# Kernel optimization log

Hardware: AMD Instinct MI355X
Metric: run time of the kernel (lower is better)

The kernel has to match this reference:

```python
import jax, jax.numpy as jnp
import numpy as np

N = 1_000_000
FEAT_DIM = 256
N_CLASS = 345
N_DOMAIN = 6
BETA = 0.5
EPS = 1e-5


def setup_inputs() -> dict:
    key = jax.random.key(0)
    k1, k2, k3, k4 = jax.random.split(key, 4)
    feats = jax.random.normal(k1, (N, FEAT_DIM), dtype=jnp.float32)
    mean = jax.random.normal(k2, (N_DOMAIN, N_CLASS, FEAT_DIM), dtype=jnp.float32)
    amount = jnp.zeros((N_DOMAIN, N_CLASS), dtype=jnp.float32)
    labels = jax.random.randint(k3, (N,), 0, N_CLASS, dtype=jnp.int64 if jax.config.jax_enable_x64 else jnp.int32)
    domains = jax.random.randint(k4, (N,), 0, N_DOMAIN, dtype=jnp.int64 if jax.config.jax_enable_x64 else jnp.int32)
    return {"feats": feats, "mean": mean, "amount": amount,
            "labels": labels, "domains": domains}


def reference(feats, mean, amount, labels, domains):
    # Segmented per-(domain, class) mean of feats. Equivalent to the original
    # onehot broadcast-multiply + sum, but without the O(N*C*F) intermediate.
    seg = domains * N_CLASS + labels  # [N]
    sums = jax.ops.segment_sum(feats, seg, num_segments=N_DOMAIN * N_CLASS)
    sums = sums.reshape(N_DOMAIN, N_CLASS, FEAT_DIM)
    counts = jax.ops.segment_sum(jnp.ones((feats.shape[0],), dtype=feats.dtype), seg,
                                 num_segments=N_DOMAIN * N_CLASS)
    counts = counts.reshape(N_DOMAIN, N_CLASS)

    tmp_mean = sums / (counts[..., None] + EPS)  # [D, C, F]
    # Mask of (domain, class) cells actually observed (tmp_mean row nonzero)
    tmp_mask = (jnp.sum(tmp_mean, axis=-1) != 0).astype(feats.dtype)[..., None]  # [D, C, 1]

    new_mean = mean * (1.0 - tmp_mask) + (mean * BETA + tmp_mean * (1.0 - BETA)) * tmp_mask
    new_amount = jnp.where(counts > 0, jnp.ones_like(amount), amount)
    return new_mean, new_amount
```

## Files before the change

kernel.cpp:

```cpp
#include <hip/hip_runtime.h>
#include <stddef.h>

constexpr int FEAT = 256;
constexpr int F4   = FEAT / 4;
constexpr int NCLS = 345;
constexpr int NDOM = 6;
constexpr int NSEG = NCLS * NDOM;
constexpr int SB   = 256;
constexpr int ITILE = 1024;
constexpr float BETA = 0.5f;
constexpr float EPS  = 1e-5f;

typedef float f32x4 __attribute__((ext_vector_type(4)));

__global__ void __launch_bounds__(256)
k_seg_hist(const int* __restrict__ labels, const int* __restrict__ domains,
           int n, int chunk, int* __restrict__ seg, int* __restrict__ W) {
    __shared__ int h[NSEG];
    for (int i = threadIdx.x; i < NSEG; i += blockDim.x) h[i] = 0;
    __syncthreads();
    const int b  = blockIdx.x;
    const int lo = b * chunk;
    const int hi = min(n, lo + chunk);
    for (int i = lo + threadIdx.x; i < hi; i += blockDim.x) {
        int s = domains[i] * NCLS + labels[i];
        seg[i] = s;
        atomicAdd(&h[s], 1);
    }
    __syncthreads();
    int* Wb = W + (size_t)b * NSEG;
    for (int i = threadIdx.x; i < NSEG; i += blockDim.x) Wb[i] = h[i];
}

__global__ void k_totals(const int* __restrict__ W, int* __restrict__ totals) {
    const int s = blockIdx.x;
    const int t = threadIdx.x;
    int sum = 0;
    for (int b = t; b < SB; b += 64) sum += W[(size_t)b * NSEG + s];
    for (int off = 1; off < 64; off <<= 1) sum += __shfl_xor(sum, off, 64);
    if (t == 0) totals[s] = sum;
}

__global__ void k_scan(const int* __restrict__ totals, int* __restrict__ offsets,
                       int* __restrict__ ticket) {
    constexpr int T  = 256;
    constexpr int CH = (NSEG + T - 1) / T;
    __shared__ int csum[T];
    int t = threadIdx.x;
    if (t == 0) ticket[0] = 0;
    int base = t * CH;
    int sum = 0;
    for (int j = 0; j < CH; ++j) {
        int idx = base + j;
        if (idx < NSEG) sum += totals[idx];
    }
    csum[t] = sum;
    __syncthreads();
    for (int off = 1; off < T; off <<= 1) {
        int v = (t >= off) ? csum[t - off] : 0;
        __syncthreads();
        csum[t] += v;
        __syncthreads();
    }
    int run = csum[t] - sum;
    for (int j = 0; j < CH; ++j) {
        int idx = base + j;
        if (idx < NSEG) {
            offsets[idx] = run;
            run += totals[idx];
        }
    }
}

__global__ void __launch_bounds__(256)
k_bases(const int* __restrict__ W, const int* __restrict__ offsets,
        int* __restrict__ Bmat) {
    const int s = blockIdx.x;
    const int t = threadIdx.x;
    __shared__ int sc[SB];
    int w = W[(size_t)t * NSEG + s];
    sc[t] = w;
    __syncthreads();
    for (int off = 1; off < SB; off <<= 1) {
        int v = (t >= off) ? sc[t - off] : 0;
        __syncthreads();
        sc[t] += v;
        __syncthreads();
    }
    Bmat[(size_t)t * NSEG + s] = offsets[s] + (sc[t] - w);
}

__global__ void __launch_bounds__(256)
k_scatter(const int* __restrict__ seg, int n, int chunk,
          const int* __restrict__ Bmat, int* __restrict__ sorted) {
    __shared__ int cur[NSEG];
    const int b = blockIdx.x;
    const int* Bb = Bmat + (size_t)b * NSEG;
    for (int i = threadIdx.x; i < NSEG; i += blockDim.x) cur[i] = Bb[i];
    __syncthreads();
    const int lo = b * chunk;
    const int hi = min(n, lo + chunk);
    for (int i = lo + threadIdx.x; i < hi; i += blockDim.x) {
        int s = seg[i];
        int pos = atomicAdd(&cur[s], 1);
        sorted[pos] = i;
    }
}

__global__ void __launch_bounds__(256)
k_reduce(const float* __restrict__ feats, const float* __restrict__ mean,
         const float* __restrict__ amount, const int* __restrict__ sorted,
         const int* __restrict__ counts, const int* __restrict__ offsets,
         int* __restrict__ ticket, float* __restrict__ out) {
    __shared__ int   idx[ITILE];
    __shared__ f32x4 sh[4][F4];
    __shared__ int   s_seg;
    const int lane = threadIdx.x & 63;
    const int rp   = threadIdx.x >> 6;

    for (;;) {
        if (threadIdx.x == 0) s_seg = atomicAdd(ticket, 1);
        __syncthreads();
        const int seg = s_seg;
        if (seg >= NSEG) break;
        const int cnt  = counts[seg];
        const int base = offsets[seg];

        f32x4 acc = (f32x4)0.0f;
        for (int t0 = 0; t0 < cnt; t0 += ITILE) {
            const int tile = min(ITILE, cnt - t0);
            for (int i = threadIdx.x; i < tile; i += 256) idx[i] = sorted[base + t0 + i];
            __syncthreads();
            int r = rp;
            for (; r + 28 < tile; r += 32) {
                int i0 = idx[r];      int i1 = idx[r + 4];
                int i2 = idx[r + 8];  int i3 = idx[r + 12];
                int i4 = idx[r + 16]; int i5 = idx[r + 20];
                int i6 = idx[r + 24]; int i7 = idx[r + 28];
                f32x4 v0 = __builtin_nontemporal_load(reinterpret_cast<const f32x4*>(feats + (size_t)i0 * FEAT) + lane);
                f32x4 v1 = __builtin_nontemporal_load(reinterpret_cast<const f32x4*>(feats + (size_t)i1 * FEAT) + lane);
                f32x4 v2 = __builtin_nontemporal_load(reinterpret_cast<const f32x4*>(feats + (size_t)i2 * FEAT) + lane);
                f32x4 v3 = __builtin_nontemporal_load(reinterpret_cast<const f32x4*>(feats + (size_t)i3 * FEAT) + lane);
                f32x4 v4 = __builtin_nontemporal_load(reinterpret_cast<const f32x4*>(feats + (size_t)i4 * FEAT) + lane);
                f32x4 v5 = __builtin_nontemporal_load(reinterpret_cast<const f32x4*>(feats + (size_t)i5 * FEAT) + lane);
                f32x4 v6 = __builtin_nontemporal_load(reinterpret_cast<const f32x4*>(feats + (size_t)i6 * FEAT) + lane);
                f32x4 v7 = __builtin_nontemporal_load(reinterpret_cast<const f32x4*>(feats + (size_t)i7 * FEAT) + lane);
                acc += (v0 + v1) + (v2 + v3) + ((v4 + v5) + (v6 + v7));
            }
            for (; r < tile; r += 4) {
                int i0 = idx[r];
                acc += __builtin_nontemporal_load(reinterpret_cast<const f32x4*>(feats + (size_t)i0 * FEAT) + lane);
            }
            __syncthreads();
        }

        sh[rp][lane] = acc;
        __syncthreads();
        if (rp == 0) {
            f32x4 s = acc + sh[1][lane] + sh[2][lane] + sh[3][lane];
            float inv = 1.0f / ((float)cnt + EPS);
            f32x4 tm = s * inv;

            float lsum = tm.x + tm.y + tm.z + tm.w;
            for (int off = 1; off < 64; off <<= 1) lsum += __shfl_xor(lsum, off, 64);
            bool msk = (lsum != 0.0f);

            f32x4 m4 = reinterpret_cast<const f32x4*>(mean)[(size_t)seg * F4 + lane];
            f32x4 o = msk ? (m4 * BETA + tm * (1.0f - BETA)) : m4;
            reinterpret_cast<f32x4*>(out)[(size_t)seg * F4 + lane] = o;
            if (lane == 0) {
                out[(size_t)NSEG * FEAT + seg] = (cnt > 0) ? 1.0f : amount[seg];
            }
        }
        __syncthreads();
    }
}

__global__ void k_fb_zero(float* __restrict__ out, int total) {
    int stride = gridDim.x * blockDim.x;
    for (int i = blockIdx.x * blockDim.x + threadIdx.x; i < total; i += stride) out[i] = 0.f;
}

__global__ void k_fb_acc(const float* __restrict__ feats, const int* __restrict__ labels,
                         const int* __restrict__ domains, int n, float* __restrict__ out) {
    int lane   = threadIdx.x & 63;
    int gwave  = (blockIdx.x * blockDim.x + threadIdx.x) >> 6;
    int nwaves = (gridDim.x * blockDim.x) >> 6;
    for (int i = gwave; i < n; i += nwaves) {
        int seg = domains[i] * NCLS + labels[i];
        const float4 v = reinterpret_cast<const float4*>(feats + (size_t)i * FEAT)[lane];
        float* dst = out + (size_t)seg * FEAT + lane * 4;
        atomicAdd(dst + 0, v.x);
        atomicAdd(dst + 1, v.y);
        atomicAdd(dst + 2, v.z);
        atomicAdd(dst + 3, v.w);
        if (lane == 0) atomicAdd(out + (size_t)NSEG * FEAT + seg, 1.0f);
    }
}

__global__ void k_fb_epi(const float* __restrict__ mean, const float* __restrict__ amount,
                         float* __restrict__ out) {
    int seg  = blockIdx.x;
    int lane = threadIdx.x;
    float cntf = out[(size_t)NSEG * FEAT + seg];
    float4 s = reinterpret_cast<float4*>(out)[(size_t)seg * F4 + lane];
    float inv = 1.0f / (cntf + EPS);
    float4 tm = make_float4(s.x * inv, s.y * inv, s.z * inv, s.w * inv);
    float lsum = tm.x + tm.y + tm.z + tm.w;
    for (int off = 1; off < 64; off <<= 1) lsum += __shfl_xor(lsum, off, 64);
    bool msk = (lsum != 0.0f);
    float4 m4 = reinterpret_cast<const float4*>(mean)[(size_t)seg * F4 + lane];
    float4 o;
    if (msk) {
        o.x = m4.x * BETA + tm.x * (1.f - BETA);
        o.y = m4.y * BETA + tm.y * (1.f - BETA);
        o.z = m4.z * BETA + tm.z * (1.f - BETA);
        o.w = m4.w * BETA + tm.w * (1.f - BETA);
    } else {
        o = m4;
    }
    reinterpret_cast<float4*>(out)[(size_t)seg * F4 + lane] = o;
    if (lane == 0) {
        out[(size_t)NSEG * FEAT + seg] = (cntf > 0.5f) ? 1.0f : amount[seg];
    }
}

extern "C" void kernel_launch(void* const* d_in, const int* in_sizes, int n_in,
                              void* d_out, int out_size, void* d_ws, size_t ws_size,
                              hipStream_t stream) {
    const float* feats   = (const float*)d_in[0];
    const float* mean    = (const float*)d_in[1];
    const float* amount  = (const float*)d_in[2];
    const int*   labels  = (const int*)d_in[3];
    const int*   domains = (const int*)d_in[4];
    float* out = (float*)d_out;
    const int n = in_sizes[3];
    const int chunk = (n + SB - 1) / SB;

    size_t need = ((size_t)n * 2 + (size_t)SB * NSEG * 2 + (size_t)NSEG * 2 + 1) * sizeof(int);
    if (ws_size >= need) {
        int* seg     = (int*)d_ws;
        int* W       = seg + n;
        int* totals  = W + (size_t)SB * NSEG;
        int* offsets = totals + NSEG;
        int* Bmat    = offsets + NSEG;
        int* sorted  = Bmat + (size_t)SB * NSEG;
        int* ticket  = sorted + n;

        k_seg_hist<<<SB, 256, 0, stream>>>(labels, domains, n, chunk, seg, W);
        k_totals<<<NSEG, 64, 0, stream>>>(W, totals);
        k_scan<<<1, 256, 0, stream>>>(totals, offsets, ticket);
        k_bases<<<NSEG, 256, 0, stream>>>(W, offsets, Bmat);
        k_scatter<<<SB, 256, 0, stream>>>(seg, n, chunk, Bmat, sorted);
        k_reduce<<<2048, 256, 0, stream>>>(feats, mean, amount, sorted, totals, offsets, ticket, out);
    } else {
        int total = NSEG * FEAT + NSEG;
        k_fb_zero<<<(total + 255) / 256, 256, 0, stream>>>(out, total);
        k_fb_acc<<<2048, 256, 0, stream>>>(feats, labels, domains, n, out);
        k_fb_epi<<<NSEG, 64, 0, stream>>>(mean, amount, out);
    }
}
```

Before: 246.9 us.

## Split sorted rows into fixed tiles with per-segment runs and atomic accumulation

The per-segment work-queue reduction is replaced by a fixed partition of the sorted index array: each block takes a contiguous tile, finds runs of equal segment IDs with a wave ballot, sums feature rows per run and atomically adds the partial sums into a zeroed accumulator. A separate final kernel then applies the mean/mask/blend epilogue. This aims to balance load evenly across blocks and drop the serial ticket dispatch, at the cost of float atomics, an extra sorted-segment array, and two more launches. Nontemporal loads become plain loads.

```diff
diff --git a/kernel.cpp b/kernel.cpp
--- a/kernel.cpp
+++ b/kernel.cpp
@@ -7,11 +7,16 @@
 constexpr int NDOM = 6;
 constexpr int NSEG = NCLS * NDOM;
 constexpr int SB   = 256;
-constexpr int ITILE = 1024;
+constexpr int MAXT = 512;
 constexpr float BETA = 0.5f;
 constexpr float EPS  = 1e-5f;
 
 typedef float f32x4 __attribute__((ext_vector_type(4)));
+
+__global__ void k_zero_accum(float* __restrict__ accum) {
+    int i = blockIdx.x * blockDim.x + threadIdx.x;
+    if (i < NSEG * F4) reinterpret_cast<f32x4*>(accum)[i] = (f32x4)0.0f;
+}
 
 __global__ void __launch_bounds__(256)
 k_seg_hist(const int* __restrict__ labels, const int* __restrict__ domains,
@@ -41,13 +46,11 @@
     if (t == 0) totals[s] = sum;
 }
 
-__global__ void k_scan(const int* __restrict__ totals, int* __restrict__ offsets,
-                       int* __restrict__ ticket) {
+__global__ void k_scan(const int* __restrict__ totals, int* __restrict__ offsets) {
     constexpr int T  = 256;
     constexpr int CH = (NSEG + T - 1) / T;
     __shared__ int csum[T];
     int t = threadIdx.x;
-    if (t == 0) ticket[0] = 0;
     int base = t * CH;
     int sum = 0;
     for (int j = 0; j < CH; ++j) {
@@ -92,7 +95,8 @@
 
 __global__ void __launch_bounds__(256)
 k_scatter(const int* __restrict__ seg, int n, int chunk,
-          const int* __restrict__ Bmat, int* __restrict__ sorted) {
+          const int* __restrict__ Bmat, int* __restrict__ sorted,
+          int* __restrict__ sseg) {
     __shared__ int cur[NSEG];
     const int b = blockIdx.x;
     const int* Bb = Bmat + (size_t)b * NSEG;
@@ -104,75 +108,88 @@
         int s = seg[i];
         int pos = atomicAdd(&cur[s], 1);
         sorted[pos] = i;
-    }
-}
-
-__global__ void __launch_bounds__(256)
-k_reduce(const float* __restrict__ feats, const float* __restrict__ mean,
-         const float* __restrict__ amount, const int* __restrict__ sorted,
-         const int* __restrict__ counts, const int* __restrict__ offsets,
-         int* __restrict__ ticket, float* __restrict__ out) {
-    __shared__ int   idx[ITILE];
-    __shared__ f32x4 sh[4][F4];
-    __shared__ int   s_seg;
+        sseg[pos]   = s;
+    }
+}
+
+__global__ void __launch_bounds__(256)
+k_partial(const float* __restrict__ feats, const int* __restrict__ sorted,
+          const int* __restrict__ sseg, int n, int tpt,
+          float* __restrict__ accum) {
+    __shared__ int idx[MAXT];
+    __shared__ int ssg[MAXT];
+    const int t  = blockIdx.x;
+    const int lo = t * tpt;
+    const int hi = min(n, lo + tpt);
+    const int len = hi - lo;
+    if (len <= 0) return;
+    for (int i = threadIdx.x; i < len; i += 256) {
+        idx[i] = sorted[lo + i];
+        ssg[i] = sseg[lo + i];
+    }
+    __syncthreads();
+
     const int lane = threadIdx.x & 63;
     const int rp   = threadIdx.x >> 6;
-
-    for (;;) {
-        if (threadIdx.x == 0) s_seg = atomicAdd(ticket, 1);
-        __syncthreads();
-        const int seg = s_seg;
-        if (seg >= NSEG) break;
-        const int cnt  = counts[seg];
-        const int base = offsets[seg];
-
+    const int per  = (len + 3) >> 2;
+    const int r0 = rp * per;
+    const int r1 = min(len, r0 + per);
+
+    int r = r0;
+    while (r < r1) {
+        const int cs = ssg[r];
+        int e = r;
+        for (;;) {
+            int p = e + lane;
+            int v = (p < r1) ? ssg[p] : (cs + 1);
+            unsigned long long m = __ballot(v != cs);
+            if (m) { e += (int)(__ffsll((long long)m) - 1); break; }
+            e += 64;
+        }
         f32x4 acc = (f32x4)0.0f;
-        for (int t0 = 0; t0 < cnt; t0 += ITILE) {
-            const int tile = min(ITILE, cnt - t0);
-            for (int i = threadIdx.x; i < tile; i += 256) idx[i] = sorted[base + t0 + i];
-            __syncthreads();
-            int r = rp;
-            for (; r + 28 < tile; r += 32) {
-                int i0 = idx[r];      int i1 = idx[r + 4];
-                int i2 = idx[r + 8];  int i3 = idx[r + 12];
-                int i4 = idx[r + 16]; int i5 = idx[r + 20];
-                int i6 = idx[r + 24]; int i7 = idx[r + 28];
-                f32x4 v0 = __builtin_nontemporal_load(reinterpret_cast<const f32x4*>(feats + (size_t)i0 * FEAT) + lane);
-                f32x4 v1 = __builtin_nontemporal_load(reinterpret_cast<const f32x4*>(feats + (size_t)i1 * FEAT) + lane);
-                f32x4 v2 = __builtin_nontemporal_load(reinterpret_cast<const f32x4*>(feats + (size_t)i2 * FEAT) + lane);
-                f32x4 v3 = __builtin_nontemporal_load(reinterpret_cast<const f32x4*>(feats + (size_t)i3 * FEAT) + lane);
-                f32x4 v4 = __builtin_nontemporal_load(reinterpret_cast<const f32x4*>(feats + (size_t)i4 * FEAT) + lane);
-                f32x4 v5 = __builtin_nontemporal_load(reinterpret_cast<const f32x4*>(feats + (size_t)i5 * FEAT) + lane);
-                f32x4 v6 = __builtin_nontemporal_load(reinterpret_cast<const f32x4*>(feats + (size_t)i6 * FEAT) + lane);
-                f32x4 v7 = __builtin_nontemporal_load(reinterpret_cast<const f32x4*>(feats + (size_t)i7 * FEAT) + lane);
-                acc += (v0 + v1) + (v2 + v3) + ((v4 + v5) + (v6 + v7));
-            }
-            for (; r < tile; r += 4) {
-                int i0 = idx[r];
-                acc += __builtin_nontemporal_load(reinterpret_cast<const f32x4*>(feats + (size_t)i0 * FEAT) + lane);
-            }
-            __syncthreads();
-        }
-
-        sh[rp][lane] = acc;
-        __syncthreads();
-        if (rp == 0) {
-            f32x4 s = acc + sh[1][lane] + sh[2][lane] + sh[3][lane];
-            float inv = 1.0f / ((float)cnt + EPS);
-            f32x4 tm = s * inv;
-
-            float lsum = tm.x + tm.y + tm.z + tm.w;
-            for (int off = 1; off < 64; off <<= 1) lsum += __shfl_xor(lsum, off, 64);
-            bool msk = (lsum != 0.0f);
-
-            f32x4 m4 = reinterpret_cast<const f32x4*>(mean)[(size_t)seg * F4 + lane];
-            f32x4 o = msk ? (m4 * BETA + tm * (1.0f - BETA)) : m4;
-            reinterpret_cast<f32x4*>(out)[(size_t)seg * F4 + lane] = o;
-            if (lane == 0) {
-                out[(size_t)NSEG * FEAT + seg] = (cnt > 0) ? 1.0f : amount[seg];
-            }
-        }
-        __syncthreads();
+        int rr = r;
+        for (; rr + 7 < e; rr += 8) {
+            f32x4 v0 = reinterpret_cast<const f32x4*>(feats + (size_t)idx[rr    ] * FEAT)[lane];
+            f32x4 v1 = reinterpret_cast<const f32x4*>(feats + (size_t)idx[rr + 1] * FEAT)[lane];
+            f32x4 v2 = reinterpret_cast<const f32x4*>(feats + (size_t)idx[rr + 2] * FEAT)[lane];
+            f32x4 v3 = reinterpret_cast<const f32x4*>(feats + (size_t)idx[rr + 3] * FEAT)[lane];
+            f32x4 v4 = reinterpret_cast<const f32x4*>(feats + (size_t)idx[rr + 4] * FEAT)[lane];
+            f32x4 v5 = reinterpret_cast<const f32x4*>(feats + (size_t)idx[rr + 5] * FEAT)[lane];
+            f32x4 v6 = reinterpret_cast<const f32x4*>(feats + (size_t)idx[rr + 6] * FEAT)[lane];
+            f32x4 v7 = reinterpret_cast<const f32x4*>(feats + (size_t)idx[rr + 7] * FEAT)[lane];
+            acc += (v0 + v1) + (v2 + v3) + ((v4 + v5) + (v6 + v7));
+        }
+        for (; rr < e; ++rr) {
+            acc += reinterpret_cast<const f32x4*>(feats + (size_t)idx[rr] * FEAT)[lane];
+        }
+        float* dst = accum + (size_t)cs * FEAT + lane * 4;
+        atomicAdd(dst + 0, acc.x);
+        atomicAdd(dst + 1, acc.y);
+        atomicAdd(dst + 2, acc.z);
+        atomicAdd(dst + 3, acc.w);
+        r = e;
+    }
+}
+
+__global__ void k_final(const float* __restrict__ accum, const float* __restrict__ mean,
+                        const float* __restrict__ amount, const int* __restrict__ totals,
+                        float* __restrict__ out) {
+    const int seg  = blockIdx.x;
+    const int lane = threadIdx.x;
+    const int cnt  = totals[seg];
+    f32x4 s = reinterpret_cast<const f32x4*>(accum)[(size_t)seg * F4 + lane];
+    float inv = 1.0f / ((float)cnt + EPS);
+    f32x4 tm = s * inv;
+
+    float lsum = tm.x + tm.y + tm.z + tm.w;
+    for (int off = 1; off < 64; off <<= 1) lsum += __shfl_xor(lsum, off, 64);
+    bool msk = (lsum != 0.0f);
+
+    f32x4 m4 = reinterpret_cast<const f32x4*>(mean)[(size_t)seg * F4 + lane];
+    f32x4 o = msk ? (m4 * BETA + tm * (1.0f - BETA)) : m4;
+    reinterpret_cast<f32x4*>(out)[(size_t)seg * F4 + lane] = o;
+    if (lane == 0) {
+        out[(size_t)NSEG * FEAT + seg] = (cnt > 0) ? 1.0f : amount[seg];
     }
 }
 
@@ -237,7 +254,12 @@
     const int n = in_sizes[3];
     const int chunk = (n + SB - 1) / SB;
 
-    size_t need = ((size_t)n * 2 + (size_t)SB * NSEG * 2 + (size_t)NSEG * 2 + 1) * sizeof(int);
+    int grid_p = 2048;
+    int tpt    = (n + grid_p - 1) / grid_p;
+    if (tpt > MAXT) { tpt = MAXT; grid_p = (n + MAXT - 1) / MAXT; }
+
+    size_t need = ((size_t)n * 3 + (size_t)SB * NSEG * 2 + (size_t)NSEG * 2
+                   + (size_t)NSEG * FEAT) * sizeof(int);
     if (ws_size >= need) {
         int* seg     = (int*)d_ws;
         int* W       = seg + n;
@@ -245,14 +267,17 @@
         int* offsets = totals + NSEG;
         int* Bmat    = offsets + NSEG;
         int* sorted  = Bmat + (size_t)SB * NSEG;
-        int* ticket  = sorted + n;
-
+        int* sseg    = sorted + n;
+        float* accum = (float*)(sseg + n);
+
+        k_zero_accum<<<(NSEG * F4 + 255) / 256, 256, 0, stream>>>(accum);
         k_seg_hist<<<SB, 256, 0, stream>>>(labels, domains, n, chunk, seg, W);
         k_totals<<<NSEG, 64, 0, stream>>>(W, totals);
-        k_scan<<<1, 256, 0, stream>>>(totals, offsets, ticket);
+        k_scan<<<1, 256, 0, stream>>>(totals, offsets);
         k_bases<<<NSEG, 256, 0, stream>>>(W, offsets, Bmat);
-        k_scatter<<<SB, 256, 0, stream>>>(seg, n, chunk, Bmat, sorted);
-        k_reduce<<<2048, 256, 0, stream>>>(feats, mean, amount, sorted, totals, offsets, ticket, out);
+        k_scatter<<<SB, 256, 0, stream>>>(seg, n, chunk, Bmat, sorted, sseg);
+        k_partial<<<grid_p, 256, 0, stream>>>(feats, sorted, sseg, n, tpt, accum);
+        k_final<<<NSEG, 64, 0, stream>>>(accum, mean, amount, totals, out);
     } else {
         int total = NSEG * FEAT + NSEG;
         k_fb_zero<<<(total + 255) / 256, 256, 0, stream>>>(out, total);
```

Result: slower. 267.7 us (+8.4%).
